# Kernel tuning notes

Measured on AMD Instinct MI355X. Metric: run time of the kernel, lower is better.

Reference implementation:

```python
import jax, jax.numpy as jnp
import numpy as np

D_MODEL = 1024
N_HEADS = 16
D_FF = 4096
WINDOW = 256
EPS = 1e-5


def setup_inputs() -> dict:
    key = jax.random.key(0)
    ks = jax.random.split(key, 12)
    B, T, C = 4, 1024, D_MODEL
    s = lambda fan: 1.0 / np.sqrt(fan)
    return {
        "x": jax.random.normal(ks[0], (B, T, C), jnp.float32),
        "Wqkv": jax.random.normal(ks[1], (3 * C, C), jnp.float32) * s(C),
        "bqkv": jnp.zeros((3 * C,), jnp.float32),
        "Wo": jax.random.normal(ks[2], (C, C), jnp.float32) * s(C),
        "bo": jnp.zeros((C,), jnp.float32),
        "W1": jax.random.normal(ks[3], (D_FF, C), jnp.float32) * s(C),
        "b1": jnp.zeros((D_FF,), jnp.float32),
        "W2": jax.random.normal(ks[4], (C, D_FF), jnp.float32) * s(D_FF),
        "b2": jnp.zeros((C,), jnp.float32),
        "g1": jnp.ones((C,), jnp.float32),
        "be1": jnp.zeros((C,), jnp.float32),
        "g2": jnp.ones((C,), jnp.float32),
        "be2": jnp.zeros((C,), jnp.float32),
    }


def _layernorm(x, g, b):
    mu = jnp.mean(x, axis=-1, keepdims=True)
    var = jnp.mean(jnp.square(x - mu), axis=-1, keepdims=True)
    return (x - mu) * jax.lax.rsqrt(var + EPS) * g + b


def reference(x, Wqkv, bqkv, Wo, bo, W1, b1, W2, b2, g1, be1, g2, be2):
    B, T, C = x.shape
    H, Dh = N_HEADS, C // N_HEADS
    # QKV projection (torch MultiheadAttention packed in_proj)
    qkv = jnp.einsum("btc,ec->bte", x, Wqkv) + bqkv  # [B,T,3C]
    q, k, v = jnp.split(qkv, 3, axis=-1)
    q = q.reshape(B, T, H, Dh).transpose(0, 2, 1, 3)  # [B,H,T,Dh]
    k = k.reshape(B, T, H, Dh).transpose(0, 2, 1, 3)
    v = v.reshape(B, T, H, Dh).transpose(0, 2, 1, 3)
    scores = jnp.einsum("bhqd,bhkd->bhqk", q, k) / jnp.sqrt(jnp.float32(Dh))
    # causal banded mask: key j visible to query i iff 0 <= i-j < WINDOW
    i = jnp.arange(T)[:, None]
    j = jnp.arange(T)[None, :]
    band = (j <= i) & (i - j < WINDOW)
    scores = jnp.where(band, scores, -jnp.inf)
    attn = jax.nn.softmax(scores, axis=-1)
    ctx = jnp.einsum("bhqk,bhkd->bhqd", attn, v)  # [B,H,T,Dh]
    ctx = ctx.transpose(0, 2, 1, 3).reshape(B, T, C)
    attn_out = jnp.einsum("btc,oc->bto", ctx, Wo) + bo
    x = _layernorm(x + attn_out, g1, be1)
    h = jax.nn.gelu(jnp.einsum("btc,fc->btf", x, W1) + b1, approximate=False)
    ffn_out = jnp.einsum("btf,cf->btc", h, W2) + b2
    return _layernorm(x + ffn_out, g2, be2)
```

## Files before the change

kernel.cpp:

```cpp
#include <hip/hip_runtime.h>
#include <hip/hip_bf16.h>

typedef __attribute__((ext_vector_type(4))) float floatx4;
typedef __attribute__((ext_vector_type(8))) short shortx8;

struct bf4 { __hip_bfloat16 h[4]; };
union U8 { shortx8 v; __hip_bfloat16 h[8]; };

__device__ __forceinline__ void async_copy16(const __hip_bfloat16* g, __hip_bfloat16* l) {
  __builtin_amdgcn_global_load_lds((__attribute__((address_space(1))) void*)g,
                                   (__attribute__((address_space(3))) void*)l,
                                   16, 0, 0);
}

__global__ __launch_bounds__(256) void cast_kernel(const float* __restrict__ in,
                                                   __hip_bfloat16* __restrict__ out) {
  const int i = blockIdx.x * 256 + threadIdx.x;
  const float4 v = ((const float4*)in)[i];
  bf4 o4;
  o4.h[0] = __float2bfloat16(v.x);
  o4.h[1] = __float2bfloat16(v.y);
  o4.h[2] = __float2bfloat16(v.z);
  o4.h[3] = __float2bfloat16(v.w);
  *(bf4*)(out + (size_t)i * 4) = o4;
}


#define GEMM_STAGE(buf, koff)                                      \
  async_copy16(Ag0 + (koff),           &As[buf][tid * 8]);         \
  async_copy16(Ag0 + (koff) + rstride, &As[buf][tid * 8 + 2048]);  \
  async_copy16(Bg0 + (koff),           &Bs[buf][tid * 8]);         \
  async_copy16(Bg0 + (koff) + rstride, &Bs[buf][tid * 8 + 2048]);

#define GEMM_KLOOP(NI)                                                        \
  GEMM_STAGE(0, 0)                                                            \
  for (int it = 0; it < (NI); ++it) {                                         \
    const int cur = it & 1;                                                   \
    if (it + 1 < (NI)) {                                                      \
      GEMM_STAGE(cur ^ 1, (it + 1) * 32)                                      \
      asm volatile("s_waitcnt vmcnt(4)" ::: "memory");                        \
    } else {                                                                  \
      asm volatile("s_waitcnt vmcnt(0)" ::: "memory");                        \
    }                                                                         \
    asm volatile("s_barrier" ::: "memory");                                   \
    const __hip_bfloat16* Ac = As[cur];                                       \
    const __hip_bfloat16* Bc = Bs[cur];                                       \
    shortx8 afr[4], bfr[4];                                                   \
    _Pragma("unroll")                                                         \
    for (int i = 0; i < 4; ++i) {                                             \
      afr[i] = *(const shortx8*)&Ac[(wr * 64 + i * 16 + fr) * 32 + sw];       \
      bfr[i] = *(const shortx8*)&Bc[(wc * 64 + i * 16 + fr) * 32 + sw];       \
    }                                                                         \
    _Pragma("unroll")                                                         \
    for (int mi = 0; mi < 4; ++mi)                                            \
      _Pragma("unroll")                                                       \
      for (int ni = 0; ni < 4; ++ni)                                          \
        acc[mi][ni] = __builtin_amdgcn_mfma_f32_16x16x32_bf16(                \
            afr[mi], bfr[ni], acc[mi][ni], 0, 0, 0);                          \
    asm volatile("s_barrier" ::: "memory");                                   \
  }

template<int EPI>
__global__ __launch_bounds__(256) void gemm_bt(
    const __hip_bfloat16* __restrict__ A,
    const __hip_bfloat16* __restrict__ B,
    const float* __restrict__ bias,
    __hip_bfloat16* __restrict__ outb,
    int M, int N, int K)
{
  __shared__ __align__(16) __hip_bfloat16 As[2][128 * 32];
  __shared__ __align__(16) __hip_bfloat16 Bs[2][128 * 32];
  const int tid  = threadIdx.x;
  const int lane = tid & 63;
  const int wave = tid >> 6;
  const int wr = wave >> 1, wc = wave & 1;
  const long bm = (long)blockIdx.y * 128, bn = (long)blockIdx.x * 128;

  const int srow = tid >> 2;
  const int scol = ((((tid & 3) - (tid >> 3)) & 3) << 3);
  const __hip_bfloat16* Ag0 = A + (bm + srow) * (long)K + scol;
  const __hip_bfloat16* Bg0 = B + (bn + srow) * (long)K + scol;
  const long rstride = 64l * K;

  const int fr = lane & 15;
  const int fq = lane >> 4;
  const int sw = (((fq + ((fr >> 1) & 3)) & 3) << 3);

  const floatx4 zero = {0.f, 0.f, 0.f, 0.f};
  floatx4 acc[4][4];
#pragma unroll
  for (int mi = 0; mi < 4; ++mi)
#pragma unroll
    for (int ni = 0; ni < 4; ++ni) acc[mi][ni] = zero;

  const int NI = K >> 5;
  GEMM_KLOOP(NI)

#pragma unroll
  for (int mi = 0; mi < 4; ++mi) {
#pragma unroll
    for (int ni = 0; ni < 4; ++ni) {
      const long col = bn + wc * 64 + ni * 16 + fr;
      const float bv = bias[col];
#pragma unroll
      for (int r = 0; r < 4; ++r) {
        const long row = bm + wr * 64 + mi * 16 + fq * 4 + r;
        float v = acc[mi][ni][r] + bv;
        if (EPI == 1) {
          const float u = v + 0.044715f * v * v * v;
          v = v / (1.0f + __expf(-1.5957691216057308f * u));
        }
        outb[(size_t)row * N + col] = __float2bfloat16(v);
      }
    }
  }
}

__global__ __launch_bounds__(256) void gemm_bt_splitk(
    const __hip_bfloat16* __restrict__ A,
    const __hip_bfloat16* __restrict__ B,
    float* __restrict__ part,
    int M, int N, int K, int Klen)
{
  __shared__ __align__(16) __hip_bfloat16 As[2][128 * 32];
  __shared__ __align__(16) __hip_bfloat16 Bs[2][128 * 32];
  const int tid  = threadIdx.x;
  const int lane = tid & 63;
  const int wave = tid >> 6;
  const int wr = wave >> 1, wc = wave & 1;
  const long bm = (long)blockIdx.y * 128, bn = (long)blockIdx.x * 128;
  const int kstart = blockIdx.z * Klen;

  const int srow = tid >> 2;
  const int scol = ((((tid & 3) - (tid >> 3)) & 3) << 3);
  const __hip_bfloat16* Ag0 = A + (bm + srow) * (long)K + kstart + scol;
  const __hip_bfloat16* Bg0 = B + (bn + srow) * (long)K + kstart + scol;
  const long rstride = 64l * K;

  const int fr = lane & 15;
  const int fq = lane >> 4;
  const int sw = (((fq + ((fr >> 1) & 3)) & 3) << 3);

  const floatx4 zero = {0.f, 0.f, 0.f, 0.f};
  floatx4 acc[4][4];
#pragma unroll
  for (int mi = 0; mi < 4; ++mi)
#pragma unroll
    for (int ni = 0; ni < 4; ++ni) acc[mi][ni] = zero;

  const int NI = Klen >> 5;
  GEMM_KLOOP(NI)

  float* outp = part + (size_t)blockIdx.z * M * N;
#pragma unroll
  for (int mi = 0; mi < 4; ++mi) {
#pragma unroll
    for (int ni = 0; ni < 4; ++ni) {
      const long col = bn + wc * 64 + ni * 16 + fr;
#pragma unroll
      for (int r = 0; r < 4; ++r) {
        const long row = bm + wr * 64 + mi * 16 + fq * 4 + r;
        outp[(size_t)row * N + col] = acc[mi][ni][r];
      }
    }
  }
}

__global__ __launch_bounds__(256) void transpose_v_kernel(
    const __hip_bfloat16* __restrict__ qkv, __hip_bfloat16* __restrict__ vt)
{
  const int bh = blockIdx.y;
  const int tt = blockIdx.x;
  const int b = bh >> 4, h = bh & 15;
  __shared__ __hip_bfloat16 tile[64][65];
  const int tid = threadIdx.x;
  const int r = tid >> 2;
  const int c = (tid & 3) << 4;
  const __hip_bfloat16* src = qkv + (size_t)(b * 1024 + tt * 64 + r) * 3072 + 2048 + h * 64 + c;
  U8 u0, u1;
  u0.v = *(const shortx8*)src;
  u1.v = *(const shortx8*)(src + 8);
#pragma unroll
  for (int j = 0; j < 8; ++j) { tile[r][c + j] = u0.h[j]; tile[r][c + 8 + j] = u1.h[j]; }
  __syncthreads();
  U8 w0, w1;
#pragma unroll
  for (int j = 0; j < 8; ++j) { w0.h[j] = tile[c + j][r]; w1.h[j] = tile[c + 8 + j][r]; }
  __hip_bfloat16* dst = vt + ((size_t)bh * 64 + r) * 1024 + tt * 64 + c;
  *(shortx8*)dst       = w0.v;
  *(shortx8*)(dst + 8) = w1.v;
}

__global__ __launch_bounds__(256) void attn_kernel(
    const __hip_bfloat16* __restrict__ qkv,
    const __hip_bfloat16* __restrict__ vt,
    __hip_bfloat16* __restrict__ ctx)
{
  const int wave = threadIdx.x >> 6;
  const int lane = threadIdx.x & 63;
  const int gw = blockIdx.x * 4 + wave;
  const int qt = gw & 63;
  const int bh = gw >> 6;
  const int b = bh >> 4, h = bh & 15;
  const int fr = lane & 15, fq = lane >> 4;
  const int q0 = qt << 4;

  __shared__ __align__(16) __hip_bfloat16 Plds[4][16 * 32];
  __hip_bfloat16* Pw = Plds[wave];

  const __hip_bfloat16* qrow = qkv + (size_t)(b * 1024 + q0 + fr) * 3072 + h * 64;
  const shortx8 aq0 = *(const shortx8*)(qrow + fq * 8);
  const shortx8 aq1 = *(const shortx8*)(qrow + 32 + fq * 8);

  const float SC = 0.125f * 1.44269504088896f;
  float m_r[4] = {-1e30f, -1e30f, -1e30f, -1e30f};
  float l_r[4] = {0.f, 0.f, 0.f, 0.f};
  const floatx4 zero = {0.f, 0.f, 0.f, 0.f};
  floatx4 o[4];
#pragma unroll
  for (int nd = 0; nd < 4; ++nd) o[nd] = zero;

  const int kt0 = (q0 >= 255) ? ((q0 - 255) >> 5) : 0;
  const int kt1 = (q0 + 15) >> 5;
  for (int kt = kt0; kt <= kt1; ++kt) {
    const int kbase = kt << 5;
    const __hip_bfloat16* krow0 = qkv + (size_t)(b * 1024 + kbase + fr) * 3072 + 1024 + h * 64;
    const __hip_bfloat16* krow1 = krow0 + 16 * 3072;
    const shortx8 bk00 = *(const shortx8*)(krow0 + fq * 8);
    const shortx8 bk01 = *(const shortx8*)(krow0 + 32 + fq * 8);
    const shortx8 bk10 = *(const shortx8*)(krow1 + fq * 8);
    const shortx8 bk11 = *(const shortx8*)(krow1 + 32 + fq * 8);
    floatx4 s0 = zero, s1 = zero;
    s0 = __builtin_amdgcn_mfma_f32_16x16x32_bf16(aq0, bk00, s0, 0, 0, 0);
    s0 = __builtin_amdgcn_mfma_f32_16x16x32_bf16(aq1, bk01, s0, 0, 0, 0);
    s1 = __builtin_amdgcn_mfma_f32_16x16x32_bf16(aq0, bk10, s1, 0, 0, 0);
    s1 = __builtin_amdgcn_mfma_f32_16x16x32_bf16(aq1, bk11, s1, 0, 0, 0);
#pragma unroll
    for (int r = 0; r < 4; ++r) { s0[r] *= SC; s1[r] *= SC; }
    if (kbase + 31 > q0 || kbase < q0 - 240) {
#pragma unroll
      for (int r = 0; r < 4; ++r) {
        const int tq = q0 + fq * 4 + r;
        const int j0 = kbase + fr;
        const int j1 = j0 + 16;
        if (j0 > tq || j0 < tq - 255) s0[r] = -3e38f;
        if (j1 > tq || j1 < tq - 255) s1[r] = -3e38f;
      }
    }
#pragma unroll
    for (int r = 0; r < 4; ++r) {
      float vmax = fmaxf(s0[r], s1[r]);
      vmax = fmaxf(vmax, __shfl_xor(vmax, 1));
      vmax = fmaxf(vmax, __shfl_xor(vmax, 2));
      vmax = fmaxf(vmax, __shfl_xor(vmax, 4));
      vmax = fmaxf(vmax, __shfl_xor(vmax, 8));
      const float mnew = fmaxf(m_r[r], vmax);
      const float alpha = exp2f(m_r[r] - mnew);
      const float p0 = exp2f(s0[r] - mnew);
      const float p1 = exp2f(s1[r] - mnew);
      m_r[r] = mnew;
      float ps = p0 + p1;
      ps += __shfl_xor(ps, 1);
      ps += __shfl_xor(ps, 2);
      ps += __shfl_xor(ps, 4);
      ps += __shfl_xor(ps, 8);
      l_r[r] = l_r[r] * alpha + ps;
      o[0][r] *= alpha; o[1][r] *= alpha; o[2][r] *= alpha; o[3][r] *= alpha;
      Pw[(fq * 4 + r) * 32 + fr]      = __float2bfloat16(p0);
      Pw[(fq * 4 + r) * 32 + 16 + fr] = __float2bfloat16(p1);
    }
    asm volatile("s_waitcnt lgkmcnt(0)" ::: "memory");
    const shortx8 ap = *(const shortx8*)&Pw[fr * 32 + fq * 8];
#pragma unroll
    for (int nd = 0; nd < 4; ++nd) {
      const shortx8 bv = *(const shortx8*)&vt[((size_t)bh * 64 + nd * 16 + fr) * 1024 + kbase + fq * 8];
      o[nd] = __builtin_amdgcn_mfma_f32_16x16x32_bf16(ap, bv, o[nd], 0, 0, 0);
    }
    asm volatile("s_waitcnt lgkmcnt(0)" ::: "memory");
  }
#pragma unroll
  for (int nd = 0; nd < 4; ++nd)
#pragma unroll
    for (int r = 0; r < 4; ++r)
      ctx[(size_t)(b * 1024 + q0 + fq * 4 + r) * 1024 + h * 64 + nd * 16 + fr] =
          __float2bfloat16(o[nd][r] / l_r[r]);
}

template<int S, int WB>
__global__ __launch_bounds__(256) void ln_sum_kernel(
    const float* __restrict__ part,
    const float* __restrict__ resid,
    const float* __restrict__ bias,
    const float* __restrict__ g, const float* __restrict__ be,
    float* __restrict__ outf, __hip_bfloat16* __restrict__ outb)
{
  const int row = blockIdx.x;
  const int tid = threadIdx.x;
  const size_t base = (size_t)row * 1024;
  float4 v = ((const float4*)(resid + base))[tid];
  const float4 bv = ((const float4*)bias)[tid];
  v.x += bv.x; v.y += bv.y; v.z += bv.z; v.w += bv.w;
#pragma unroll
  for (int s = 0; s < S; ++s) {
    const float4 p = ((const float4*)(part + (size_t)s * 4096 * 1024 + base))[tid];
    v.x += p.x; v.y += p.y; v.z += p.z; v.w += p.w;
  }
  float sm  = v.x + v.y + v.z + v.w;
  float ss = v.x * v.x + v.y * v.y + v.z * v.z + v.w * v.w;
#pragma unroll
  for (int off = 1; off < 64; off <<= 1) {
    sm += __shfl_xor(sm, off);
    ss += __shfl_xor(ss, off);
  }
  __shared__ float red[8];
  if ((tid & 63) == 0) { red[tid >> 6] = sm; red[4 + (tid >> 6)] = ss; }
  __syncthreads();
  sm = red[0] + red[1] + red[2] + red[3];
  ss = red[4] + red[5] + red[6] + red[7];
  const float mu = sm * (1.0f / 1024.0f);
  const float rs = rsqrtf(ss * (1.0f / 1024.0f) - mu * mu + 1e-5f);
  const float4 gg = ((const float4*)g)[tid];
  const float4 bb = ((const float4*)be)[tid];
  float4 y;
  y.x = (v.x - mu) * rs * gg.x + bb.x;
  y.y = (v.y - mu) * rs * gg.y + bb.y;
  y.z = (v.z - mu) * rs * gg.z + bb.z;
  y.w = (v.w - mu) * rs * gg.w + bb.w;
  ((float4*)(outf + base))[tid] = y;
  if (WB) {
    bf4 o4;
    o4.h[0] = __float2bfloat16(y.x);
    o4.h[1] = __float2bfloat16(y.y);
    o4.h[2] = __float2bfloat16(y.z);
    o4.h[3] = __float2bfloat16(y.w);
    *(bf4*)(outb + base + tid * 4) = o4;
  }
}

extern "C" void kernel_launch(void* const* d_in, const int* in_sizes, int n_in,
                              void* d_out, int out_size, void* d_ws, size_t ws_size,
                              hipStream_t stream) {
  const float* x    = (const float*)d_in[0];
  const float* Wqkv = (const float*)d_in[1];
  const float* bqkv = (const float*)d_in[2];
  const float* Wo   = (const float*)d_in[3];
  const float* bo   = (const float*)d_in[4];
  const float* W1   = (const float*)d_in[5];
  const float* b1   = (const float*)d_in[6];
  const float* W2   = (const float*)d_in[7];
  const float* b2   = (const float*)d_in[8];
  const float* g1   = (const float*)d_in[9];
  const float* be1  = (const float*)d_in[10];
  const float* g2   = (const float*)d_in[11];
  const float* be2  = (const float*)d_in[12];

  char* ws = (char*)d_ws;
  size_t off = 0;
  auto alloc = [&](size_t bytes) -> void* {
    void* p = ws + off;
    off += (bytes + 255) & ~(size_t)255;
    return p;
  };
  __hip_bfloat16* wbuf = (__hip_bfloat16*)alloc(8u << 20);
  __hip_bfloat16* xb   = (__hip_bfloat16*)alloc(8388608);
  __hip_bfloat16* qkvb = (__hip_bfloat16*)alloc(25165824);
  __hip_bfloat16* vtb  = (__hip_bfloat16*)alloc(8388608);
  __hip_bfloat16* ctxb = (__hip_bfloat16*)alloc(8388608);
  float*          part = (float*)alloc(4u * 16777216);
  float*          x1f  = (float*)alloc(16777216);
  __hip_bfloat16* x1b  = (__hip_bfloat16*)alloc(8388608);
  __hip_bfloat16* hb   = (__hip_bfloat16*)alloc(33554432);
  (void)ws_size; (void)in_sizes; (void)n_in; (void)out_size;

  cast_kernel<<<4096, 256, 0, stream>>>(x, xb);
  cast_kernel<<<3072, 256, 0, stream>>>(Wqkv, wbuf);
  gemm_bt<0><<<dim3(24, 32), 256, 0, stream>>>(xb, wbuf, bqkv, qkvb, 4096, 3072, 1024);
  transpose_v_kernel<<<dim3(16, 64), 256, 0, stream>>>(qkvb, vtb);
  attn_kernel<<<1024, 256, 0, stream>>>(qkvb, vtb, ctxb);
  cast_kernel<<<1024, 256, 0, stream>>>(Wo, wbuf);
  gemm_bt_splitk<<<dim3(8, 32, 2), 256, 0, stream>>>(ctxb, wbuf, part, 4096, 1024, 1024, 512);
  ln_sum_kernel<2, 1><<<4096, 256, 0, stream>>>(part, x, bo, g1, be1, x1f, x1b);
  cast_kernel<<<4096, 256, 0, stream>>>(W1, wbuf);
  gemm_bt<1><<<dim3(32, 32), 256, 0, stream>>>(x1b, wbuf, b1, hb, 4096, 4096, 1024);
  cast_kernel<<<4096, 256, 0, stream>>>(W2, wbuf);
  gemm_bt_splitk<<<dim3(8, 32, 4), 256, 0, stream>>>(hb, wbuf, part, 4096, 1024, 4096, 1024);
  ln_sum_kernel<4, 0><<<4096, 256, 0, stream>>>(part, x1f, b2, g2, be2, (float*)d_out, nullptr);
}
```

Measured before the change: 369.2 us.

## Merge weight casts, swizzle GEMM tiles per XCD, store split-K partials as bf16

All five fp32-to-bf16 casts now run in a single kernel launch, with separate destination buffers per weight, which removes four launches. Both GEMM kernels remap the flat block index so that consecutive blocks on the same XCD share M-tiles, aiming for better L2 reuse. Split-K partial sums are written and read as bf16 instead of fp32, halving partial-buffer traffic. The cost is lower precision in the summed partials before layernorm.

```diff
diff --git a/kernel.cpp b/kernel.cpp
--- a/kernel.cpp
+++ b/kernel.cpp
@@ -6,6 +6,7 @@
 
 struct bf4 { __hip_bfloat16 h[4]; };
 union U8 { shortx8 v; __hip_bfloat16 h[8]; };
+union U4 { unsigned long long v; __hip_bfloat16 h[4]; };
 
 __device__ __forceinline__ void async_copy16(const __hip_bfloat16* g, __hip_bfloat16* l) {
   __builtin_amdgcn_global_load_lds((__attribute__((address_space(1))) void*)g,
@@ -13,18 +14,43 @@
                                    16, 0, 0);
 }
 
-__global__ __launch_bounds__(256) void cast_kernel(const float* __restrict__ in,
-                                                   __hip_bfloat16* __restrict__ out) {
-  const int i = blockIdx.x * 256 + threadIdx.x;
-  const float4 v = ((const float4*)in)[i];
+__global__ __launch_bounds__(256) void cast_all_kernel(
+    const float* __restrict__ s0, __hip_bfloat16* __restrict__ d0, int nb0,
+    const float* __restrict__ s1, __hip_bfloat16* __restrict__ d1, int nb1,
+    const float* __restrict__ s2, __hip_bfloat16* __restrict__ d2, int nb2,
+    const float* __restrict__ s3, __hip_bfloat16* __restrict__ d3, int nb3,
+    const float* __restrict__ s4, __hip_bfloat16* __restrict__ d4) {
+  int b = blockIdx.x;
+  const float* src; __hip_bfloat16* dst;
+  if (b < nb0) { src = s0; dst = d0; }
+  else { b -= nb0;
+    if (b < nb1) { src = s1; dst = d1; }
+    else { b -= nb1;
+      if (b < nb2) { src = s2; dst = d2; }
+      else { b -= nb2;
+        if (b < nb3) { src = s3; dst = d3; }
+        else { b -= nb3; src = s4; dst = d4; }
+      }
+    }
+  }
+  const int i = b * 256 + threadIdx.x;
+  const float4 v = ((const float4*)src)[i];
   bf4 o4;
   o4.h[0] = __float2bfloat16(v.x);
   o4.h[1] = __float2bfloat16(v.y);
   o4.h[2] = __float2bfloat16(v.z);
   o4.h[3] = __float2bfloat16(v.w);
-  *(bf4*)(out + (size_t)i * 4) = o4;
-}
-
+  *(bf4*)(dst + (size_t)i * 4) = o4;
+}
+
+#define GEMM_SWIZZLE()                                                        \
+  const int flat = blockIdx.x + gridDim.x * (blockIdx.y + 32 * blockIdx.z);   \
+  const int xcd_ = flat & 7;                                                  \
+  int rsw_ = flat >> 3;                                                       \
+  const int mt_ = xcd_ * 4 + (rsw_ & 3);                                      \
+  rsw_ >>= 2;                                                                 \
+  const int nt_ = rsw_ % gridDim.x;                                           \
+  const int zt_ = rsw_ / gridDim.x;
 
 #define GEMM_STAGE(buf, koff)                                      \
   async_copy16(Ag0 + (koff),           &As[buf][tid * 8]);         \
@@ -74,7 +100,9 @@
   const int lane = tid & 63;
   const int wave = tid >> 6;
   const int wr = wave >> 1, wc = wave & 1;
-  const long bm = (long)blockIdx.y * 128, bn = (long)blockIdx.x * 128;
+  GEMM_SWIZZLE()
+  const long bm = (long)mt_ * 128, bn = (long)nt_ * 128;
+  (void)zt_;
 
   const int srow = tid >> 2;
   const int scol = ((((tid & 3) - (tid >> 3)) & 3) << 3);
@@ -119,7 +147,7 @@
 __global__ __launch_bounds__(256) void gemm_bt_splitk(
     const __hip_bfloat16* __restrict__ A,
     const __hip_bfloat16* __restrict__ B,
-    float* __restrict__ part,
+    __hip_bfloat16* __restrict__ part,
     int M, int N, int K, int Klen)
 {
   __shared__ __align__(16) __hip_bfloat16 As[2][128 * 32];
@@ -128,8 +156,9 @@
   const int lane = tid & 63;
   const int wave = tid >> 6;
   const int wr = wave >> 1, wc = wave & 1;
-  const long bm = (long)blockIdx.y * 128, bn = (long)blockIdx.x * 128;
-  const int kstart = blockIdx.z * Klen;
+  GEMM_SWIZZLE()
+  const long bm = (long)mt_ * 128, bn = (long)nt_ * 128;
+  const int kstart = zt_ * Klen;
 
   const int srow = tid >> 2;
   const int scol = ((((tid & 3) - (tid >> 3)) & 3) << 3);
@@ -151,7 +180,7 @@
   const int NI = Klen >> 5;
   GEMM_KLOOP(NI)
 
-  float* outp = part + (size_t)blockIdx.z * M * N;
+  __hip_bfloat16* outp = part + (size_t)zt_ * M * N;
 #pragma unroll
   for (int mi = 0; mi < 4; ++mi) {
 #pragma unroll
@@ -160,7 +189,7 @@
 #pragma unroll
       for (int r = 0; r < 4; ++r) {
         const long row = bm + wr * 64 + mi * 16 + fq * 4 + r;
-        outp[(size_t)row * N + col] = acc[mi][ni][r];
+        outp[(size_t)row * N + col] = __float2bfloat16(acc[mi][ni][r]);
       }
     }
   }
@@ -288,7 +317,7 @@
 
 template<int S, int WB>
 __global__ __launch_bounds__(256) void ln_sum_kernel(
-    const float* __restrict__ part,
+    const __hip_bfloat16* __restrict__ part,
     const float* __restrict__ resid,
     const float* __restrict__ bias,
     const float* __restrict__ g, const float* __restrict__ be,
@@ -302,10 +331,14 @@
   v.x += bv.x; v.y += bv.y; v.z += bv.z; v.w += bv.w;
 #pragma unroll
   for (int s = 0; s < S; ++s) {
-    const float4 p = ((const float4*)(part + (size_t)s * 4096 * 1024 + base))[tid];
-    v.x += p.x; v.y += p.y; v.z += p.z; v.w += p.w;
-  }
-  float sm  = v.x + v.y + v.z + v.w;
+    U4 p;
+    p.v = *(const unsigned long long*)&part[(size_t)s * 4096 * 1024 + base + tid * 4];
+    v.x += __bfloat162float(p.h[0]);
+    v.y += __bfloat162float(p.h[1]);
+    v.z += __bfloat162float(p.h[2]);
+    v.w += __bfloat162float(p.h[3]);
+  }
+  float sm = v.x + v.y + v.z + v.w;
   float ss = v.x * v.x + v.y * v.y + v.z * v.z + v.w * v.w;
 #pragma unroll
   for (int off = 1; off < 64; off <<= 1) {
@@ -361,28 +394,31 @@
     off += (bytes + 255) & ~(size_t)255;
     return p;
   };
-  __hip_bfloat16* wbuf = (__hip_bfloat16*)alloc(8u << 20);
-  __hip_bfloat16* xb   = (__hip_bfloat16*)alloc(8388608);
-  __hip_bfloat16* qkvb = (__hip_bfloat16*)alloc(25165824);
-  __hip_bfloat16* vtb  = (__hip_bfloat16*)alloc(8388608);
-  __hip_bfloat16* ctxb = (__hip_bfloat16*)alloc(8388608);
-  float*          part = (float*)alloc(4u * 16777216);
-  float*          x1f  = (float*)alloc(16777216);
-  __hip_bfloat16* x1b  = (__hip_bfloat16*)alloc(8388608);
-  __hip_bfloat16* hb   = (__hip_bfloat16*)alloc(33554432);
+  __hip_bfloat16* wqkvb = (__hip_bfloat16*)alloc(6291456);
+  __hip_bfloat16* wob   = (__hip_bfloat16*)alloc(2097152);
+  __hip_bfloat16* w1b   = (__hip_bfloat16*)alloc(8388608);
+  __hip_bfloat16* w2b   = (__hip_bfloat16*)alloc(8388608);
+  __hip_bfloat16* xb    = (__hip_bfloat16*)alloc(8388608);
+  __hip_bfloat16* qkvb  = (__hip_bfloat16*)alloc(25165824);
+  __hip_bfloat16* vtb   = (__hip_bfloat16*)alloc(8388608);
+  __hip_bfloat16* ctxb  = (__hip_bfloat16*)alloc(8388608);
+  __hip_bfloat16* part  = (__hip_bfloat16*)alloc(4u * 8388608);
+  float*          x1f   = (float*)alloc(16777216);
+  __hip_bfloat16* x1b   = (__hip_bfloat16*)alloc(8388608);
+  __hip_bfloat16* hb    = (__hip_bfloat16*)alloc(33554432);
   (void)ws_size; (void)in_sizes; (void)n_in; (void)out_size;
 
-  cast_kernel<<<4096, 256, 0, stream>>>(x, xb);
-  cast_kernel<<<3072, 256, 0, stream>>>(Wqkv, wbuf);
-  gemm_bt<0><<<dim3(24, 32), 256, 0, stream>>>(xb, wbuf, bqkv, qkvb, 4096, 3072, 1024);
+  cast_all_kernel<<<16384, 256, 0, stream>>>(x, xb, 4096,
+                                             Wqkv, wqkvb, 3072,
+                                             Wo, wob, 1024,
+                                             W1, w1b, 4096,
+                                             W2, w2b);
+  gemm_bt<0><<<dim3(24, 32), 256, 0, stream>>>(xb, wqkvb, bqkv, qkvb, 4096, 3072, 1024);
   transpose_v_kernel<<<dim3(16, 64), 256, 0, stream>>>(qkvb, vtb);
   attn_kernel<<<1024, 256, 0, stream>>>(qkvb, vtb, ctxb);
-  cast_kernel<<<1024, 256, 0, stream>>>(Wo, wbuf);
-  gemm_bt_splitk<<<dim3(8, 32, 2), 256, 0, stream>>>(ctxb, wbuf, part, 4096, 1024, 1024, 512);
+  gemm_bt_splitk<<<dim3(8, 32, 2), 256, 0, stream>>>(ctxb, wob, part, 4096, 1024, 1024, 512);
   ln_sum_kernel<2, 1><<<4096, 256, 0, stream>>>(part, x, bo, g1, be1, x1f, x1b);
-  cast_kernel<<<4096, 256, 0, stream>>>(W1, wbuf);
-  gemm_bt<1><<<dim3(32, 32), 256, 0, stream>>>(x1b, wbuf, b1, hb, 4096, 4096, 1024);
-  cast_kernel<<<4096, 256, 0, stream>>>(W2, wbuf);
-  gemm_bt_splitk<<<dim3(8, 32, 4), 256, 0, stream>>>(hb, wbuf, part, 4096, 1024, 4096, 1024);
+  gemm_bt<1><<<dim3(32, 32), 256, 0, stream>>>(x1b, w1b, b1, hb, 4096, 4096, 1024);
+  gemm_bt_splitk<<<dim3(8, 32, 4), 256, 0, stream>>>(hb, w2b, part, 4096, 1024, 4096, 1024);
   ln_sum_kernel<4, 0><<<4096, 256, 0, stream>>>(part, x1f, b2, g2, be2, (float*)d_out, nullptr);
 }
```

After: 359.3 us. -2.7%, faster.
